# Kernel optimization log

Hardware: AMD Instinct MI355X
Metric: run time of the kernel (lower is better)

Reference implementation:

```python
import jax, jax.numpy as jnp
import numpy as np

B, H, W, C = 8, 64, 64, 256
NH, WS, SS = 8, 8, 4
HD = C // NH          # head dim 32
N = WS * WS           # 64 tokens per window
NW = (H // WS) * (W // WS)  # 64 windows
MLP = 4 * C


def _rel_index():
    ch = np.arange(WS)
    coords = np.stack(np.meshgrid(ch, ch, indexing='ij')).reshape(2, -1)  # [2, N]
    rel = (coords[:, :, None] - coords[:, None, :]).transpose(1, 2, 0)   # [N, N, 2]
    rel[:, :, 0] += WS - 1
    rel[:, :, 1] += WS - 1
    rel[:, :, 0] *= 2 * WS - 1
    return jnp.asarray(rel.sum(-1))  # [N, N] indices into table

REL_IDX = _rel_index()


def _attn_mask():
    # standard Swin shifted-window mask: [nW, N, N] with 0 / -100
    img = np.zeros((H, W))
    slices = (slice(0, -WS), slice(-WS, -SS), slice(-SS, None))
    cnt = 0
    for hs in slices:
        for ws_ in slices:
            img[hs, ws_] = cnt
            cnt += 1
    m = img.reshape(H // WS, WS, W // WS, WS).transpose(0, 2, 1, 3).reshape(-1, N)
    diff = m[:, None, :] - m[:, :, None]
    return jnp.asarray(np.where(diff != 0, -100.0, 0.0).astype(np.float32))

MASK = _attn_mask()


def setup_inputs() -> dict:
    key = jax.random.key(0)
    ks = jax.random.split(key, 8)
    s = 0.02
    return {
        'hidden_states': jax.random.normal(ks[0], (B, H * W, C), jnp.float32),
        'ln1_g': jnp.ones((C,), jnp.float32),
        'ln1_b': jnp.zeros((C,), jnp.float32),
        'wq': jax.random.normal(ks[1], (C, C), jnp.float32) * s,
        'bq': jnp.zeros((C,), jnp.float32),
        'wk': jax.random.normal(ks[2], (C, C), jnp.float32) * s,
        'bk': jnp.zeros((C,), jnp.float32),
        'wv': jax.random.normal(ks[3], (C, C), jnp.float32) * s,
        'bv': jnp.zeros((C,), jnp.float32),
        'rel_table': jax.random.normal(ks[4], ((2 * WS - 1) ** 2, NH), jnp.float32) * s,
        'wo': jax.random.normal(ks[5], (C, C), jnp.float32) * s,
        'bo': jnp.zeros((C,), jnp.float32),
        'ln2_g': jnp.ones((C,), jnp.float32),
        'ln2_b': jnp.zeros((C,), jnp.float32),
        'w1': jax.random.normal(ks[6], (MLP, C), jnp.float32) * s,
        'b1': jnp.zeros((MLP,), jnp.float32),
        'w2': jax.random.normal(ks[7], (C, MLP), jnp.float32) * s,
        'b2': jnp.zeros((C,), jnp.float32),
    }


def _ln(x, g, b):
    mu = x.mean(-1, keepdims=True)
    var = x.var(-1, keepdims=True)
    return (x - mu) * jax.lax.rsqrt(var + 1e-5) * g + b


def reference(hidden_states, ln1_g, ln1_b, wq, bq, wk, bk, wv, bv, rel_table,
              wo, bo, ln2_g, ln2_b, w1, b1, w2, b2):
    shortcut = hidden_states
    x = _ln(hidden_states, ln1_g, ln1_b).reshape(B, H, W, C)
    # cyclic shift
    x = jnp.roll(x, (-SS, -SS), axis=(1, 2))
    # window partition -> [B*nW, N, C]
    xw = x.reshape(B, H // WS, WS, W // WS, WS, C).transpose(0, 1, 3, 2, 4, 5).reshape(-1, N, C)
    q = (xw @ wq.T + bq).reshape(-1, N, NH, HD).transpose(0, 2, 1, 3)
    k = (xw @ wk.T + bk).reshape(-1, N, NH, HD).transpose(0, 2, 1, 3)
    v = (xw @ wv.T + bv).reshape(-1, N, NH, HD).transpose(0, 2, 1, 3)
    scores = jnp.einsum('bhnd,bhmd->bhnm', q, k) / np.float32(np.sqrt(HD))
    bias = rel_table[REL_IDX]                 # [N, N, NH] gathered bias
    scores = scores + bias.transpose(2, 0, 1)[None]
    scores = scores.reshape(B, NW, NH, N, N) + MASK[None, :, None]
    probs = jax.nn.softmax(scores, axis=-1).reshape(-1, NH, N, N)
    ctx = jnp.einsum('bhnm,bhmd->bnhd', probs, v).reshape(-1, N, C)
    attn_out = ctx @ wo.T + bo                # SelfOutput dense
    # window reverse + reverse shift
    x = attn_out.reshape(B, H // WS, W // WS, WS, WS, C).transpose(0, 1, 3, 2, 4, 5).reshape(B, H, W, C)
    x = jnp.roll(x, (SS, SS), axis=(1, 2)).reshape(B, H * W, C)
    hidden = shortcut + x
    y = _ln(hidden, ln2_g, ln2_b)
    y = jax.nn.gelu(y @ w1.T + b1, approximate=False) @ w2.T + b2
    return hidden + y
```

## Files before the change

### kernel.cpp

```cpp
#include <hip/hip_runtime.h>
#include <hip/hip_bf16.h>
#include <math.h>

__device__ __forceinline__ unsigned short f2bf(float f) {
    union { float f; unsigned u; } c; c.f = f;
    unsigned r = c.u + 0x7fffu + ((c.u >> 16) & 1u);
    return (unsigned short)(r >> 16);
}

typedef __bf16 bf16x8_t __attribute__((ext_vector_type(8)));
typedef float  f32x4_t  __attribute__((ext_vector_type(4)));

#define AS1 __attribute__((address_space(1)))
#define AS3 __attribute__((address_space(3)))
__device__ __forceinline__ void g2lds16(const void* g, void* l) {
    __builtin_amdgcn_global_load_lds((const AS1 unsigned int*)g, (AS3 unsigned int*)l, 16, 0, 0);
}

__global__ void cvt_all(const float* __restrict__ wq, const float* __restrict__ wk,
                        const float* __restrict__ wv, const float* __restrict__ wo,
                        const float* __restrict__ w1, const float* __restrict__ w2,
                        unsigned short* __restrict__ wqkv_b, unsigned short* __restrict__ wo_b,
                        unsigned short* __restrict__ w1_b, unsigned short* __restrict__ w2_b) {
    int i = blockIdx.x * 256 + threadIdx.x;
    const float* src; unsigned short* dst; int base;
    if (i < 16384)       { src = wq; dst = wqkv_b;          base = 0; }
    else if (i < 32768)  { src = wk; dst = wqkv_b + 65536;  base = 16384; }
    else if (i < 49152)  { src = wv; dst = wqkv_b + 131072; base = 32768; }
    else if (i < 65536)  { src = wo; dst = wo_b;            base = 49152; }
    else if (i < 131072) { src = w1; dst = w1_b;            base = 65536; }
    else                 { src = w2; dst = w2_b;            base = 131072; }
    int j = (i - base) * 4;
    float4 v = *(const float4*)(src + j);
    ushort4 o = { f2bf(v.x), f2bf(v.y), f2bf(v.z), f2bf(v.w) };
    *(ushort4*)(dst + j) = o;
}

template<int GATHER>
__global__ void ln_kernel(const float* __restrict__ x, const float* __restrict__ g,
                          const float* __restrict__ b, unsigned short* __restrict__ out) {
    int row  = blockIdx.x * 4 + (threadIdx.x >> 6);
    int lane = threadIdx.x & 63;
    int src;
    if (GATHER) {
        int bb = row >> 12;
        int rem = row & 4095;
        int winid = rem >> 6, tok = rem & 63;
        int wi = winid >> 3, wj = winid & 7;
        int ii = tok >> 3,  jj = tok & 7;
        int hh = (wi * 8 + ii + 4) & 63;
        int ww = (wj * 8 + jj + 4) & 63;
        src = (bb << 12) + hh * 64 + ww;
    } else {
        src = row;
    }
    const float4 v = *(const float4*)(x + (size_t)src * 256 + lane * 4);
    float s  = v.x + v.y + v.z + v.w;
    float s2 = v.x*v.x + v.y*v.y + v.z*v.z + v.w*v.w;
    #pragma unroll
    for (int off = 32; off > 0; off >>= 1) {
        s  += __shfl_xor(s,  off, 64);
        s2 += __shfl_xor(s2, off, 64);
    }
    float mean = s * (1.0f / 256.0f);
    float var  = s2 * (1.0f / 256.0f) - mean * mean;
    float rstd = rsqrtf(var + 1e-5f);
    int c0 = lane * 4;
    float4 gg  = *(const float4*)(g + c0);
    float4 bb4 = *(const float4*)(b + c0);
    ushort4 o;
    o.x = f2bf((v.x - mean) * rstd * gg.x + bb4.x);
    o.y = f2bf((v.y - mean) * rstd * gg.y + bb4.y);
    o.z = f2bf((v.z - mean) * rstd * gg.z + bb4.z);
    o.w = f2bf((v.w - mean) * rstd * gg.w + bb4.w);
    *(ushort4*)(out + (size_t)row * 256 + c0) = o;
}

template<int MODE>
__global__ __launch_bounds__(256) void gemm_tile(
        const unsigned short* __restrict__ A,
        const unsigned short* __restrict__ Bw,
        const float* __restrict__ bias,
        int M, int N, int K,
        unsigned short* __restrict__ obf,
        float* __restrict__ of32,
        const float* __restrict__ addf) {
    __shared__ unsigned short As[128 * 32];
    __shared__ unsigned short Bs[128 * 32];
    int t = threadIdx.x;
    int lane = t & 63, wave = t >> 6;
    int m0 = blockIdx.x * 128, n0 = blockIdx.y * 128;
    int wm = (wave >> 1) * 64, wn = (wave & 1) * 64;
    int lr = lane & 15, kg = lane >> 4;

    f32x4_t acc[4][4];
    #pragma unroll
    for (int i = 0; i < 4; ++i)
        #pragma unroll
        for (int j = 0; j < 4; ++j) { acc[i][j][0]=0.f; acc[i][j][1]=0.f; acc[i][j][2]=0.f; acc[i][j][3]=0.f; }

    int srow = t >> 2, schunk = (t & 3) * 8;
    const unsigned short* ga0 = A  + (size_t)(m0 + srow)      * K + schunk;
    const unsigned short* ga1 = A  + (size_t)(m0 + 64 + srow) * K + schunk;
    const unsigned short* gb0 = Bw + (size_t)(n0 + srow)      * K + schunk;
    const unsigned short* gb1 = Bw + (size_t)(n0 + 64 + srow) * K + schunk;
    unsigned short* la0 = &As[t * 8];
    unsigned short* la1 = &As[2048 + t * 8];
    unsigned short* lb0 = &Bs[t * 8];
    unsigned short* lb1 = &Bs[2048 + t * 8];

    for (int k0 = 0; k0 < K; k0 += 32) {
        __syncthreads();
        g2lds16(ga0 + k0, la0);
        g2lds16(ga1 + k0, la1);
        g2lds16(gb0 + k0, lb0);
        g2lds16(gb1 + k0, lb1);
        __syncthreads();
        bf16x8_t af[4], bfr[4];
        #pragma unroll
        for (int i = 0; i < 4; ++i)
            af[i] = *(const bf16x8_t*)&As[(wm + i * 16 + lr) * 32 + kg * 8];
        #pragma unroll
        for (int j = 0; j < 4; ++j)
            bfr[j] = *(const bf16x8_t*)&Bs[(wn + j * 16 + lr) * 32 + kg * 8];
        #pragma unroll
        for (int i = 0; i < 4; ++i)
            #pragma unroll
            for (int j = 0; j < 4; ++j)
                acc[i][j] = __builtin_amdgcn_mfma_f32_16x16x32_bf16(af[i], bfr[j], acc[i][j], 0, 0, 0);
    }

    #pragma unroll
    for (int i = 0; i < 4; ++i) {
        #pragma unroll
        for (int j = 0; j < 4; ++j) {
            int col = n0 + wn + j * 16 + lr;
            float bv = bias[col];
            #pragma unroll
            for (int e = 0; e < 4; ++e) {
                int row = m0 + wm + i * 16 + kg * 4 + e;
                float v = acc[i][j][e] + bv;
                if (MODE == 0) {
                    obf[(size_t)row * N + col] = f2bf(v);
                } else if (MODE == 1) {
                    float gv = 0.5f * v * (1.0f + erff(v * 0.70710678118654752f));
                    obf[(size_t)row * N + col] = f2bf(gv);
                } else if (MODE == 2) {
                    int bb = row >> 12;
                    int rem = row & 4095;
                    int winid = rem >> 6, tok = rem & 63;
                    int wi = winid >> 3, wj = winid & 7;
                    int ii = tok >> 3,  jj = tok & 7;
                    int hh = (wi * 8 + ii + 4) & 63;
                    int ww = (wj * 8 + jj + 4) & 63;
                    size_t dst = ((size_t)(bb << 12) + hh * 64 + ww) * 256 + col;
                    of32[dst] = addf[dst] + v;
                } else {
                    size_t dst = (size_t)row * N + col;
                    of32[dst] = addf[dst] + v;
                }
            }
        }
    }
}

#define PR 72
#define VR 72
__global__ void __launch_bounds__(256) attn_mfma(
        const unsigned short* __restrict__ qkv,
        const float* __restrict__ relt,
        unsigned short* __restrict__ ctx) {
    __shared__ float rs[1800];
    __shared__ unsigned short Pl[4][64 * PR];
    __shared__ unsigned short Vt[4][32 * VR];

    int t = threadIdx.x;
    int lane = t & 63, wave = t >> 6;
    for (int i = t; i < 1800; i += 256) rs[i] = relt[i];
    __syncthreads();

    int wh = blockIdx.x * 4 + wave;
    int wg = wh >> 3, h = wh & 7;
    int win = wg & 63;
    int ln = lane & 15, quad = lane >> 4;

    unsigned short* P = &Pl[wave][0];
    unsigned short* V = &Vt[wave][0];
    const unsigned short* base = qkv + (size_t)wg * 64 * 768 + h * 32;

    union BF8 { bf16x8_t v; unsigned short s[8]; };
    {
        const bf16x8_t* vp = (const bf16x8_t*)(base + (size_t)lane * 768 + 512);
        BF8 vv[4];
        #pragma unroll
        for (int c = 0; c < 4; ++c) vv[c].v = vp[c];
        #pragma unroll
        for (int c = 0; c < 4; ++c)
            #pragma unroll
            for (int e = 0; e < 8; ++e)
                V[(c * 8 + e) * VR + lane] = vv[c].s[e];
    }

    bf16x8_t qa[4], kb[4];
    #pragma unroll
    for (int i = 0; i < 4; ++i)
        qa[i] = *(const bf16x8_t*)(base + (size_t)(i * 16 + ln) * 768 + quad * 8);
    #pragma unroll
    for (int j = 0; j < 4; ++j)
        kb[j] = *(const bf16x8_t*)(base + (size_t)(j * 16 + ln) * 768 + 256 + quad * 8);

    f32x4_t acc[4][4];
    #pragma unroll
    for (int i = 0; i < 4; ++i)
        #pragma unroll
        for (int j = 0; j < 4; ++j) { acc[i][j][0]=0.f; acc[i][j][1]=0.f; acc[i][j][2]=0.f; acc[i][j][3]=0.f; }
    #pragma unroll
    for (int i = 0; i < 4; ++i)
        #pragma unroll
        for (int j = 0; j < 4; ++j)
            acc[i][j] = __builtin_amdgcn_mfma_f32_16x16x32_bf16(qa[i], kb[j], acc[i][j], 0, 0, 0);

    const float scale = 0.17677669529663687f;
    int wi = win >> 3, wj = win & 7;
    int mjv = ln & 7;
    int regm[4], mi[4];
    #pragma unroll
    for (int j = 0; j < 4; ++j) {
        mi[j] = j * 2 + (ln >> 3);
        int hm = wi * 8 + mi[j], wm = wj * 8 + mjv;
        regm[j] = (hm < 56 ? 0 : (hm < 60 ? 1 : 2)) * 3 + (wm < 56 ? 0 : (wm < 60 ? 1 : 2));
    }
    float inv[4][4];
    #pragma unroll
    for (int i = 0; i < 4; ++i) {
        #pragma unroll
        for (int e = 0; e < 4; ++e) {
            int q = i * 16 + quad * 4 + e;
            int ti = q >> 3, tj = q & 7;
            int hn = wi * 8 + ti, wn = wj * 8 + tj;
            int regn = (hn < 56 ? 0 : (hn < 60 ? 1 : 2)) * 3 + (wn < 56 ? 0 : (wn < 60 ? 1 : 2));
            float sum = 0.f;
            #pragma unroll
            for (int j = 0; j < 4; ++j) {
                float bv = rs[((ti - mi[j] + 7) * 15 + (tj - mjv + 7)) * 8 + h];
                float s = acc[i][j][e] * scale + bv + (regm[j] != regn ? -100.f : 0.f);
                float p = __expf(s);
                sum += p;
                P[q * PR + j * 16 + ln] = f2bf(p);
            }
            #pragma unroll
            for (int off = 1; off < 16; off <<= 1) sum += __shfl_xor(sum, off, 64);
            inv[i][e] = 1.0f / sum;
        }
    }
    __syncthreads();

    bf16x8_t vb[2][2];
    #pragma unroll
    for (int jd = 0; jd < 2; ++jd)
        #pragma unroll
        for (int kc = 0; kc < 2; ++kc)
            vb[jd][kc] = *(const bf16x8_t*)&V[(jd * 16 + ln) * VR + kc * 32 + quad * 8];
    f32x4_t occ[4][2];
    #pragma unroll
    for (int i = 0; i < 4; ++i)
        #pragma unroll
        for (int jd = 0; jd < 2; ++jd) { occ[i][jd][0]=0.f; occ[i][jd][1]=0.f; occ[i][jd][2]=0.f; occ[i][jd][3]=0.f; }
    #pragma unroll
    for (int i = 0; i < 4; ++i) {
        #pragma unroll
        for (int kc = 0; kc < 2; ++kc) {
            bf16x8_t pf = *(const bf16x8_t*)&P[(i * 16 + ln) * PR + kc * 32 + quad * 8];
            occ[i][0] = __builtin_amdgcn_mfma_f32_16x16x32_bf16(pf, vb[0][kc], occ[i][0], 0, 0, 0);
            occ[i][1] = __builtin_amdgcn_mfma_f32_16x16x32_bf16(pf, vb[1][kc], occ[i][1], 0, 0, 0);
        }
    }

    unsigned short* cbase = ctx + (size_t)wg * 64 * 256 + h * 32;
    #pragma unroll
    for (int i = 0; i < 4; ++i)
        #pragma unroll
        for (int e = 0; e < 4; ++e) {
            int q = i * 16 + quad * 4 + e;
            #pragma unroll
            for (int jd = 0; jd < 2; ++jd)
                cbase[(size_t)q * 256 + jd * 16 + ln] = f2bf(occ[i][jd][e] * inv[i][e]);
        }
}

extern "C" void kernel_launch(void* const* d_in, const int* in_sizes, int n_in,
                              void* d_out, int out_size, void* d_ws, size_t ws_size,
                              hipStream_t stream) {
    const float* hs   = (const float*)d_in[0];
    const float* ln1g = (const float*)d_in[1];
    const float* ln1b = (const float*)d_in[2];
    const float* wq   = (const float*)d_in[3];
    const float* bq   = (const float*)d_in[4];
    const float* wk   = (const float*)d_in[5];
    const float* bk   = (const float*)d_in[6];
    const float* wv   = (const float*)d_in[7];
    const float* bv   = (const float*)d_in[8];
    const float* relt = (const float*)d_in[9];
    const float* wo   = (const float*)d_in[10];
    const float* bo   = (const float*)d_in[11];
    const float* ln2g = (const float*)d_in[12];
    const float* ln2b = (const float*)d_in[13];
    const float* w1   = (const float*)d_in[14];
    const float* b1   = (const float*)d_in[15];
    const float* w2   = (const float*)d_in[16];
    const float* b2   = (const float*)d_in[17];
    float* out = (float*)d_out;

    const size_t NTOK = 32768;
    size_t off = 0;
    auto carve = [&](size_t bytes) { void* p = (char*)d_ws + off; off += (bytes + 255) & ~(size_t)255; return p; };
    unsigned short* wqkv_b = (unsigned short*)carve(768ull * 256 * 2);
    unsigned short* wo_b   = (unsigned short*)carve(65536ull * 2);
    unsigned short* w1_b   = (unsigned short*)carve(262144ull * 2);
    unsigned short* w2_b   = (unsigned short*)carve(262144ull * 2);
    float*          bqkv   = (float*)carve(768ull * 4);
    float*          hidden = (float*)carve(NTOK * 256 * 4);
    unsigned short* xw     = (unsigned short*)carve(NTOK * 256 * 2);
    unsigned short* qkvb   = (unsigned short*)carve(NTOK * 768 * 2);
    unsigned short* cx     = (unsigned short*)carve(NTOK * 256 * 2);
    unsigned short* h1 = qkvb;
    unsigned short* yb = xw;

    cvt_all<<<768, 256, 0, stream>>>(wq, wk, wv, wo, w1, w2, wqkv_b, wo_b, w1_b, w2_b);
    hipMemcpyAsync(bqkv,       bq, 256 * 4, hipMemcpyDeviceToDevice, stream);
    hipMemcpyAsync(bqkv + 256, bk, 256 * 4, hipMemcpyDeviceToDevice, stream);
    hipMemcpyAsync(bqkv + 512, bv, 256 * 4, hipMemcpyDeviceToDevice, stream);

    ln_kernel<1><<<8192, 256, 0, stream>>>(hs, ln1g, ln1b, xw);

    gemm_tile<0><<<dim3(256, 6), 256, 0, stream>>>(xw, wqkv_b, bqkv, 32768, 768, 256, qkvb, nullptr, nullptr);

    attn_mfma<<<1024, 256, 0, stream>>>(qkvb, relt, cx);

    gemm_tile<2><<<dim3(256, 2), 256, 0, stream>>>(cx, wo_b, bo, 32768, 256, 256, nullptr, hidden, hs);

    ln_kernel<0><<<8192, 256, 0, stream>>>(hidden, ln2g, ln2b, yb);

    gemm_tile<1><<<dim3(256, 8), 256, 0, stream>>>(yb, w1_b, b1, 32768, 1024, 256, h1, nullptr, nullptr);

    gemm_tile<3><<<dim3(256, 2), 256, 0, stream>>>(h1, w2_b, b2, 32768, 256, 1024, nullptr, out, hidden);
}
```

Before: 274.3 us.

## Widen GEMM K-tile with XOR-swizzled LDS, bf16 residual, tanh GELU, constexpr K

The GEMM now stages a K tile of 64 instead of 32, with an XOR-swizzled LDS layout to avoid bank conflicts. It also takes K as a compile-time template parameter so the K loop fully unrolls, and adds an occupancy hint to launch_bounds. The intermediate residual 'hidden' is stored as bf16 instead of fp32 to halve its traffic in the Wo, LN2 and W2 stages. The exact erf GELU is replaced by a tanh/sigmoid approximation. The bf16 residual and the GELU approximation lower accuracy of the residual path.

```diff
diff --git a/kernel.cpp b/kernel.cpp
--- a/kernel.cpp
+++ b/kernel.cpp
@@ -6,6 +6,13 @@
     union { float f; unsigned u; } c; c.f = f;
     unsigned r = c.u + 0x7fffu + ((c.u >> 16) & 1u);
     return (unsigned short)(r >> 16);
+}
+__device__ __forceinline__ float bfu(unsigned short u) {
+    union { unsigned x; float f; } c; c.x = ((unsigned)u) << 16; return c.f;
+}
+__device__ __forceinline__ float gelu_t(float x) {
+    float z = x * (1.59576912f + 0.07135481f * x * x);
+    return x / (1.0f + __expf(-z));
 }
 
 typedef __bf16 bf16x8_t __attribute__((ext_vector_type(8)));
@@ -36,8 +43,8 @@
     *(ushort4*)(dst + j) = o;
 }
 
-template<int GATHER>
-__global__ void ln_kernel(const float* __restrict__ x, const float* __restrict__ g,
+template<int GATHER, int BF16IN>
+__global__ void ln_kernel(const void* __restrict__ xv, const float* __restrict__ g,
                           const float* __restrict__ b, unsigned short* __restrict__ out) {
     int row  = blockIdx.x * 4 + (threadIdx.x >> 6);
     int lane = threadIdx.x & 63;
@@ -54,7 +61,13 @@
     } else {
         src = row;
     }
-    const float4 v = *(const float4*)(x + (size_t)src * 256 + lane * 4);
+    float4 v;
+    if (BF16IN) {
+        ushort4 u = *(const ushort4*)((const unsigned short*)xv + (size_t)src * 256 + lane * 4);
+        v.x = bfu(u.x); v.y = bfu(u.y); v.z = bfu(u.z); v.w = bfu(u.w);
+    } else {
+        v = *(const float4*)((const float*)xv + (size_t)src * 256 + lane * 4);
+    }
     float s  = v.x + v.y + v.z + v.w;
     float s2 = v.x*v.x + v.y*v.y + v.z*v.z + v.w*v.w;
     #pragma unroll
@@ -76,22 +89,22 @@
     *(ushort4*)(out + (size_t)row * 256 + c0) = o;
 }
 
-template<int MODE>
-__global__ __launch_bounds__(256) void gemm_tile(
+template<int MODE, int K>
+__global__ __launch_bounds__(256, 4) void gemm_tile(
         const unsigned short* __restrict__ A,
         const unsigned short* __restrict__ Bw,
         const float* __restrict__ bias,
-        int M, int N, int K,
+        int M, int N,
         unsigned short* __restrict__ obf,
         float* __restrict__ of32,
-        const float* __restrict__ addf) {
-    __shared__ unsigned short As[128 * 32];
-    __shared__ unsigned short Bs[128 * 32];
-    int t = threadIdx.x;
-    int lane = t & 63, wave = t >> 6;
-    int m0 = blockIdx.x * 128, n0 = blockIdx.y * 128;
-    int wm = (wave >> 1) * 64, wn = (wave & 1) * 64;
-    int lr = lane & 15, kg = lane >> 4;
+        const void* __restrict__ addp) {
+    __shared__ unsigned short As[128 * 64];
+    __shared__ unsigned short Bs[128 * 64];
+    const int t = threadIdx.x;
+    const int lane = t & 63, wave = t >> 6;
+    const int m0 = blockIdx.x * 128, n0 = blockIdx.y * 128;
+    const int wm = (wave >> 1) * 64, wn = (wave & 1) * 64;
+    const int lr = lane & 15, kg = lane >> 4;
 
     f32x4_t acc[4][4];
     #pragma unroll
@@ -99,35 +112,41 @@
         #pragma unroll
         for (int j = 0; j < 4; ++j) { acc[i][j][0]=0.f; acc[i][j][1]=0.f; acc[i][j][2]=0.f; acc[i][j][3]=0.f; }
 
-    int srow = t >> 2, schunk = (t & 3) * 8;
-    const unsigned short* ga0 = A  + (size_t)(m0 + srow)      * K + schunk;
-    const unsigned short* ga1 = A  + (size_t)(m0 + 64 + srow) * K + schunk;
-    const unsigned short* gb0 = Bw + (size_t)(n0 + srow)      * K + schunk;
-    const unsigned short* gb1 = Bw + (size_t)(n0 + 64 + srow) * K + schunk;
-    unsigned short* la0 = &As[t * 8];
-    unsigned short* la1 = &As[2048 + t * 8];
-    unsigned short* lb0 = &Bs[t * 8];
-    unsigned short* lb1 = &Bs[2048 + t * 8];
-
-    for (int k0 = 0; k0 < K; k0 += 32) {
+    const int srow = t >> 3;
+    const int sc   = (((t & 7) ^ (srow & 7)) * 8);
+    const unsigned short* ga = A  + (size_t)(m0 + srow) * K + sc;
+    const unsigned short* gb = Bw + (size_t)(n0 + srow) * K + sc;
+    unsigned short* la = &As[t * 8];
+    unsigned short* lb = &Bs[t * 8];
+
+    #pragma unroll
+    for (int k0 = 0; k0 < K; k0 += 64) {
         __syncthreads();
-        g2lds16(ga0 + k0, la0);
-        g2lds16(ga1 + k0, la1);
-        g2lds16(gb0 + k0, lb0);
-        g2lds16(gb1 + k0, lb1);
+        #pragma unroll
+        for (int i = 0; i < 4; ++i) {
+            g2lds16(ga + (size_t)(i * 32) * K + k0, la + i * 2048);
+            g2lds16(gb + (size_t)(i * 32) * K + k0, lb + i * 2048);
+        }
         __syncthreads();
-        bf16x8_t af[4], bfr[4];
-        #pragma unroll
-        for (int i = 0; i < 4; ++i)
-            af[i] = *(const bf16x8_t*)&As[(wm + i * 16 + lr) * 32 + kg * 8];
-        #pragma unroll
-        for (int j = 0; j < 4; ++j)
-            bfr[j] = *(const bf16x8_t*)&Bs[(wn + j * 16 + lr) * 32 + kg * 8];
-        #pragma unroll
-        for (int i = 0; i < 4; ++i)
-            #pragma unroll
-            for (int j = 0; j < 4; ++j)
-                acc[i][j] = __builtin_amdgcn_mfma_f32_16x16x32_bf16(af[i], bfr[j], acc[i][j], 0, 0, 0);
+        #pragma unroll
+        for (int ks = 0; ks < 64; ks += 32) {
+            bf16x8_t af[4], bfr[4];
+            #pragma unroll
+            for (int i = 0; i < 4; ++i) {
+                int r = wm + i * 16 + lr;
+                af[i] = *(const bf16x8_t*)&As[r * 64 + ((((ks >> 3) + kg) ^ (r & 7)) << 3)];
+            }
+            #pragma unroll
+            for (int j = 0; j < 4; ++j) {
+                int r = wn + j * 16 + lr;
+                bfr[j] = *(const bf16x8_t*)&Bs[r * 64 + ((((ks >> 3) + kg) ^ (r & 7)) << 3)];
+            }
+            #pragma unroll
+            for (int i = 0; i < 4; ++i)
+                #pragma unroll
+                for (int j = 0; j < 4; ++j)
+                    acc[i][j] = __builtin_amdgcn_mfma_f32_16x16x32_bf16(af[i], bfr[j], acc[i][j], 0, 0, 0);
+        }
     }
 
     #pragma unroll
@@ -143,8 +162,7 @@
                 if (MODE == 0) {
                     obf[(size_t)row * N + col] = f2bf(v);
                 } else if (MODE == 1) {
-                    float gv = 0.5f * v * (1.0f + erff(v * 0.70710678118654752f));
-                    obf[(size_t)row * N + col] = f2bf(gv);
+                    obf[(size_t)row * N + col] = f2bf(gelu_t(v));
                 } else if (MODE == 2) {
                     int bb = row >> 12;
                     int rem = row & 4095;
@@ -154,10 +172,10 @@
                     int hh = (wi * 8 + ii + 4) & 63;
                     int ww = (wj * 8 + jj + 4) & 63;
                     size_t dst = ((size_t)(bb << 12) + hh * 64 + ww) * 256 + col;
-                    of32[dst] = addf[dst] + v;
+                    obf[dst] = f2bf(((const float*)addp)[dst] + v);
                 } else {
                     size_t dst = (size_t)row * N + col;
-                    of32[dst] = addf[dst] + v;
+                    of32[dst] = bfu(((const unsigned short*)addp)[dst]) + v;
                 }
             }
         }
@@ -319,7 +337,7 @@
     unsigned short* w1_b   = (unsigned short*)carve(262144ull * 2);
     unsigned short* w2_b   = (unsigned short*)carve(262144ull * 2);
     float*          bqkv   = (float*)carve(768ull * 4);
-    float*          hidden = (float*)carve(NTOK * 256 * 4);
+    unsigned short* hiddenb= (unsigned short*)carve(NTOK * 256 * 2);
     unsigned short* xw     = (unsigned short*)carve(NTOK * 256 * 2);
     unsigned short* qkvb   = (unsigned short*)carve(NTOK * 768 * 2);
     unsigned short* cx     = (unsigned short*)carve(NTOK * 256 * 2);
@@ -331,17 +349,17 @@
     hipMemcpyAsync(bqkv + 256, bk, 256 * 4, hipMemcpyDeviceToDevice, stream);
     hipMemcpyAsync(bqkv + 512, bv, 256 * 4, hipMemcpyDeviceToDevice, stream);
 
-    ln_kernel<1><<<8192, 256, 0, stream>>>(hs, ln1g, ln1b, xw);
-
-    gemm_tile<0><<<dim3(256, 6), 256, 0, stream>>>(xw, wqkv_b, bqkv, 32768, 768, 256, qkvb, nullptr, nullptr);
+    ln_kernel<1, 0><<<8192, 256, 0, stream>>>(hs, ln1g, ln1b, xw);
+
+    gemm_tile<0, 256><<<dim3(256, 6), 256, 0, stream>>>(xw, wqkv_b, bqkv, 32768, 768, qkvb, nullptr, nullptr);
 
     attn_mfma<<<1024, 256, 0, stream>>>(qkvb, relt, cx);
 
-    gemm_tile<2><<<dim3(256, 2), 256, 0, stream>>>(cx, wo_b, bo, 32768, 256, 256, nullptr, hidden, hs);
-
-    ln_kernel<0><<<8192, 256, 0, stream>>>(hidden, ln2g, ln2b, yb);
-
-    gemm_tile<1><<<dim3(256, 8), 256, 0, stream>>>(yb, w1_b, b1, 32768, 1024, 256, h1, nullptr, nullptr);
-
-    gemm_tile<3><<<dim3(256, 2), 256, 0, stream>>>(h1, w2_b, b2, 32768, 256, 1024, nullptr, out, hidden);
-}
+    gemm_tile<2, 256><<<dim3(256, 2), 256, 0, stream>>>(cx, wo_b, bo, 32768, 256, hiddenb, nullptr, hs);
+
+    ln_kernel<0, 1><<<8192, 256, 0, stream>>>(hiddenb, ln2g, ln2b, yb);
+
+    gemm_tile<1, 256><<<dim3(256, 8), 256, 0, stream>>>(yb, w1_b, b1, 32768, 1024, h1, nullptr, nullptr);
+
+    gemm_tile<3, 1024><<<dim3(256, 2), 256, 0, stream>>>(h1, w2_b, b2, 32768, 256, nullptr, out, hiddenb);
+}
```

New measurement: 290.9 us. 1.06x slower.
